# Kernel optimization log

Measured on AMD Instinct MI355X. Metric: run time of the kernel, lower is better.

Reference implementation:

```python
import jax, jax.numpy as jnp
import numpy as np

N_HEADS = 16
D_MODEL = 1024
TOTAL = 8192
N_SEQ = 8
SEQ_LEN = TOTAL // N_SEQ


def setup_inputs() -> dict:
    key = jax.random.key(0)
    ks = jax.random.split(key, 12)
    f = jnp.float32
    d = D_MODEL
    inp = {
        "query": jax.random.normal(ks[0], (TOTAL, d), f),
        "key": jax.random.normal(ks[1], (TOTAL, d), f),
        "value": jax.random.normal(ks[2], (TOTAL, d), f),
        "seq_lengths_q": jnp.full((N_SEQ,), SEQ_LEN, jnp.int64 if jax.config.jax_enable_x64 else jnp.int32),
        "seq_lengths_kv": jnp.full((N_SEQ,), SEQ_LEN, jnp.int64 if jax.config.jax_enable_x64 else jnp.int32),
        "Wq": jax.random.normal(ks[3], (d, d), f) * 0.02,
        "bq": jnp.zeros((d,), f),
        "Wk": jax.random.normal(ks[4], (d, d), f) * 0.02,
        "bk": jnp.zeros((d,), f),
        "Wv": jax.random.normal(ks[5], (d, d), f) * 0.02,
        "bv": jnp.zeros((d,), f),
        "Wo": jax.random.normal(ks[6], (d, d), f) * 0.02,
        "bo": jnpp if False else jnp.zeros((d,), f),
    }
    return inp


def reference(query, key, value, seq_lengths_q, seq_lengths_kv, Wq, bq, Wk, bk, Wv, bv, Wo, bo):
    Tq, d = query.shape
    Tkv = key.shape[0]
    H = N_HEADS
    Dh = d // H
    B = seq_lengths_q.shape[0]
    Lq = Tq // B  # equal-length packed sequences
    Lkv = Tkv // B
    scale = 1.0 / jnp.sqrt(jnp.asarray(Dh, query.dtype))

    # torch Linear: x @ W.T + b
    Q = (query @ Wq.T + bq).reshape(H, Tq, Dh)   # NOTE: raw view, no transpose
    K = (key @ Wk.T + bk).reshape(H, Tkv, Dh)    # (replicates original's view semantics)
    V = (value @ Wv.T + bv).reshape(H, Tkv, Dh)

    # Block-diagonal mask over equal-length sequences == per-block attention.
    Qb = Q.reshape(H, B, Lq, Dh)
    Kb = K.reshape(H, B, Lkv, Dh)
    Vb = V.reshape(H, B, Lkv, Dh)

    scores = jnp.einsum("hbqd,hbkd->hbqk", Qb, Kb) * scale  # [H,B,Lq,Lkv]
    probs = jax.nn.softmax(scores, axis=-1)
    attn = jnp.einsum("hbqk,hbkd->hbqd", probs, Vb)          # [H,B,Lq,Dh]

    attn = attn.reshape(H, Tq, Dh).reshape(Tq, d)  # matches .view(total_q, d_model)
    out = attn @ Wo.T + bo
    return out
```

## Files before the change

kernel.cpp:

```cpp
#include <hip/hip_runtime.h>
#include <hip/hip_bf16.h>

#define TOTAL   8192
#define DMODEL  1024
#define NHEADS  16
#define NSEQ    8
#define DH      64

typedef float  f32x4 __attribute__((ext_vector_type(4)));
typedef short  s16x8 __attribute__((ext_vector_type(8)));
typedef unsigned short u16;
typedef u16    u16x8 __attribute__((ext_vector_type(8)));

__device__ __forceinline__ u16 f2bf_rne(float x) {
  union { float f; unsigned u; } v; v.f = x;
  unsigned r = v.u + 0x7FFFu + ((v.u >> 16) & 1u);
  return (u16)(r >> 16);
}

__device__ __forceinline__ void async_cp16(const u16* g, u16* l) {
  __builtin_amdgcn_global_load_lds(
      (const __attribute__((address_space(1))) unsigned int*)g,
      (__attribute__((address_space(3))) unsigned int*)l, 16, 0, 0);
}

__device__ __forceinline__ void cvt8_one(const float* __restrict__ src,
                                         u16* __restrict__ dst, long i) {
  float4 a = *reinterpret_cast<const float4*>(src + i);
  float4 b = *reinterpret_cast<const float4*>(src + i + 4);
  u16x8 o;
  o[0] = f2bf_rne(a.x); o[1] = f2bf_rne(a.y); o[2] = f2bf_rne(a.z); o[3] = f2bf_rne(a.w);
  o[4] = f2bf_rne(b.x); o[5] = f2bf_rne(b.y); o[6] = f2bf_rne(b.z); o[7] = f2bf_rne(b.w);
  *reinterpret_cast<u16x8*>(dst + i) = o;
}

__global__ __launch_bounds__(256) void cvt8(const float* __restrict__ src,
                                            u16* __restrict__ dst) {
  cvt8_one(src, dst, ((long)blockIdx.x * 256 + threadIdx.x) * 8);
}

__global__ __launch_bounds__(256) void cvt8_w4(const float* __restrict__ w0,
                                               const float* __restrict__ w1,
                                               const float* __restrict__ w2,
                                               const float* __restrict__ w3,
                                               u16* __restrict__ dst) {
  const float* srcs[4] = {w0, w1, w2, w3};
  cvt8_one(srcs[blockIdx.y], dst + (long)blockIdx.y * (DMODEL * (long)DMODEL),
           ((long)blockIdx.x * 256 + threadIdx.x) * 8);
}

__global__ __launch_bounds__(256) void cvt8_x3(const float* __restrict__ x0,
                                               const float* __restrict__ x1,
                                               const float* __restrict__ x2,
                                               u16* __restrict__ dst) {
  const float* srcs[3] = {x0, x1, x2};
  cvt8_one(srcs[blockIdx.y], dst + (long)blockIdx.y * (TOTAL * (long)DMODEL),
           ((long)blockIdx.x * 256 + threadIdx.x) * 8);
}

template<bool OUT_BF16>
__device__ __forceinline__ void gemm_core(const u16* __restrict__ A,
                                          const u16* __restrict__ B,
                                          const float* __restrict__ bias,
                                          void* __restrict__ Cp,
                                          long bm0, long bn0,
                                          u16* As, u16* Bs) {
  const int tid  = threadIdx.x;
  const int lane = tid & 63;
  const int wv   = tid >> 6;
  const int quad = lane >> 4;
  const int m16  = lane & 15;
  const int wm   = (wv & 1) * 64;
  const int wn   = (wv >> 1) * 64;
  const int srow = lane >> 2;
  const int sk8  = (lane & 3) * 8;

  f32x4 acc[4][4] = {};
  const u16* Abase = A + bm0 * DMODEL;
  const u16* Bbase = B + bn0 * DMODEL;

  for (int k0 = 0; k0 < DMODEL; k0 += 32) {
    #pragma unroll
    for (int j = 0; j < 2; j++) {
      const int r   = j * 4 + wv;
      const int row = r * 16 + srow;
      async_cp16(Abase + (long)row * DMODEL + k0 + sk8, &As[r * 512]);
      async_cp16(Bbase + (long)row * DMODEL + k0 + sk8, &Bs[r * 512]);
    }
    __syncthreads();

    s16x8 af[4], bfr[4];
    #pragma unroll
    for (int i = 0; i < 4; i++)
      af[i] = *(const s16x8*)&As[(wm + i * 16 + m16) * 32 + quad * 8];
    #pragma unroll
    for (int j = 0; j < 4; j++)
      bfr[j] = *(const s16x8*)&Bs[(wn + j * 16 + m16) * 32 + quad * 8];
    #pragma unroll
    for (int i = 0; i < 4; i++)
      #pragma unroll
      for (int j = 0; j < 4; j++)
        acc[i][j] = __builtin_amdgcn_mfma_f32_16x16x32_bf16(af[i], bfr[j], acc[i][j], 0, 0, 0);
    __syncthreads();
  }

  #pragma unroll
  for (int j = 0; j < 4; j++) {
    const long col = bn0 + wn + j * 16 + m16;
    const float bj = bias[col];
    #pragma unroll
    for (int i = 0; i < 4; i++) {
      const long row0 = bm0 + wm + i * 16 + quad * 4;
      #pragma unroll
      for (int r = 0; r < 4; r++) {
        float v = acc[i][j][r] + bj;
        if constexpr (OUT_BF16)
          ((u16*)Cp)[(row0 + r) * DMODEL + col] = f2bf_rne(v);
        else
          ((float*)Cp)[(row0 + r) * DMODEL + col] = v;
      }
    }
  }
}

template<bool OUT_BF16>
__global__ __launch_bounds__(256) void gemm_nt_async(const u16* __restrict__ A,
                                                     const u16* __restrict__ B,
                                                     const float* __restrict__ bias,
                                                     void* __restrict__ Cp) {
  __shared__ u16 As[128 * 32];
  __shared__ u16 Bs[128 * 32];
  gemm_core<OUT_BF16>(A, B, bias, Cp,
                      (long)blockIdx.x * 128, (long)blockIdx.y * 128, As, Bs);
}

__global__ __launch_bounds__(256) void gemm_qkv(const u16* __restrict__ X3,
                                                const u16* __restrict__ W3,
                                                const float* __restrict__ bq,
                                                const float* __restrict__ bk,
                                                const float* __restrict__ bv,
                                                u16* __restrict__ QKV) {
  __shared__ u16 As[128 * 32];
  __shared__ u16 Bs[128 * 32];
  const int z = blockIdx.z;
  const float* bias = (z == 0) ? bq : (z == 1) ? bk : bv;
  gemm_core<true>(X3 + (long)z * (TOTAL * (long)DMODEL),
                  W3 + (long)z * (DMODEL * (long)DMODEL),
                  bias,
                  QKV + (long)z * (TOTAL * (long)DMODEL),
                  (long)blockIdx.x * 128, (long)blockIdx.y * 128, As, Bs);
}

__global__ __launch_bounds__(256) void transpose_v(const u16* __restrict__ Vbf,
                                                   u16* __restrict__ Vt) {
  constexpr int TP = 72;
  __shared__ u16 tile[64 * TP];
  const int tid = threadIdx.x;
  const long base = (long)blockIdx.y * 65536;
  const int kt = blockIdx.x;
  {
    int k = tid >> 2, dh0 = (tid & 3) * 16;
    const u16* g = Vbf + base + (long)(kt * 64 + k) * 64 + dh0;
    u16x8 a = ((const u16x8*)g)[0];
    u16x8 b = ((const u16x8*)g)[1];
    #pragma unroll
    for (int i = 0; i < 8; i++) tile[(dh0 + i) * TP + k] = a[i];
    #pragma unroll
    for (int i = 0; i < 8; i++) tile[(dh0 + 8 + i) * TP + k] = b[i];
  }
  __syncthreads();
  {
    int dh = tid >> 2, k0 = (tid & 3) * 16;
    u16x8 a = *(const u16x8*)&tile[dh * TP + k0];
    u16x8 b = *(const u16x8*)&tile[dh * TP + k0 + 8];
    u16* g = Vt + base + (long)dh * 1024 + kt * 64 + k0;
    ((u16x8*)g)[0] = a;
    ((u16x8*)g)[1] = b;
  }
}

__global__ __launch_bounds__(256) void attn_kernel(const u16* __restrict__ Qbf,
                                                   const u16* __restrict__ Kbf,
                                                   const u16* __restrict__ Vt,
                                                   u16* __restrict__ Obf) {
  constexpr int KP = 72;
  __shared__ u16 Ks[64 * KP];
  __shared__ u16 Vs[64 * KP];
  __shared__ u16 Es[4 * 32 * KP];
  const int tid  = threadIdx.x;
  const int lane = tid & 63;
  const int wv   = tid >> 6;
  const int quad = lane >> 4;
  const int m16  = lane & 15;
  const int qt   = blockIdx.y;
  const long base = (long)blockIdx.x * 65536;

  const int qrow0 = qt * 128 + wv * 32;
  s16x8 aq[2][2];
  #pragma unroll
  for (int g = 0; g < 2; g++)
    #pragma unroll
    for (int s = 0; s < 2; s++)
      aq[g][s] = *(const s16x8*)(Qbf + base + (long)(qrow0 + g * 16 + m16) * 64 + s * 32 + quad * 8);

  f32x4 acc_o[2][4] = {};
  f32x4 acc_d[2] = {};

  union { u16x8 u; s16x8 s; } onesu;
  u16 ov = (m16 == 0) ? (u16)0x3F80 : (u16)0;
  #pragma unroll
  for (int i = 0; i < 8; i++) onesu.u[i] = ov;
  const s16x8 bones = onesu.s;

  const float SC = 0.125f * 1.44269504088896340736f;
  const int sr = tid >> 2;
  const int sk = (tid & 3) * 16;

  for (int nt = 0; nt < 16; nt++) {
    {
      const u16* g = Kbf + base + nt * 4096 + (long)sr * 64 + sk;
      u16x8 a = ((const u16x8*)g)[0];
      u16x8 b = ((const u16x8*)g)[1];
      *(u16x8*)&Ks[sr * KP + sk]     = a;
      *(u16x8*)&Ks[sr * KP + sk + 8] = b;
    }
    {
      const u16* g = Vt + base + (long)sr * 1024 + nt * 64 + sk;
      u16x8 a = ((const u16x8*)g)[0];
      u16x8 b = ((const u16x8*)g)[1];
      *(u16x8*)&Vs[sr * KP + sk]     = a;
      *(u16x8*)&Vs[sr * KP + sk + 8] = b;
    }
    __syncthreads();

    #pragma unroll
    for (int n = 0; n < 4; n++) {
      s16x8 bk0 = *(const s16x8*)&Ks[(n * 16 + m16) * KP + quad * 8];
      s16x8 bk1 = *(const s16x8*)&Ks[(n * 16 + m16) * KP + 32 + quad * 8];
      #pragma unroll
      for (int g = 0; g < 2; g++) {
        f32x4 s = {0.f, 0.f, 0.f, 0.f};
        s = __builtin_amdgcn_mfma_f32_16x16x32_bf16(aq[g][0], bk0, s, 0, 0, 0);
        s = __builtin_amdgcn_mfma_f32_16x16x32_bf16(aq[g][1], bk1, s, 0, 0, 0);
        #pragma unroll
        for (int r = 0; r < 4; r++) {
          float e = __builtin_amdgcn_exp2f(s[r] * SC);
          Es[(wv * 32 + g * 16 + quad * 4 + r) * KP + n * 16 + m16] = f2bf_rne(e);
        }
      }
    }
    s16x8 ae[2][2];
    #pragma unroll
    for (int g = 0; g < 2; g++) {
      ae[g][0] = *(const s16x8*)&Es[(wv * 32 + g * 16 + m16) * KP + quad * 8];
      ae[g][1] = *(const s16x8*)&Es[(wv * 32 + g * 16 + m16) * KP + 32 + quad * 8];
    }
    #pragma unroll
    for (int n = 0; n < 4; n++) {
      s16x8 bv0 = *(const s16x8*)&Vs[(n * 16 + m16) * KP + quad * 8];
      s16x8 bv1 = *(const s16x8*)&Vs[(n * 16 + m16) * KP + 32 + quad * 8];
      #pragma unroll
      for (int g = 0; g < 2; g++) {
        acc_o[g][n] = __builtin_amdgcn_mfma_f32_16x16x32_bf16(ae[g][0], bv0, acc_o[g][n], 0, 0, 0);
        acc_o[g][n] = __builtin_amdgcn_mfma_f32_16x16x32_bf16(ae[g][1], bv1, acc_o[g][n], 0, 0, 0);
      }
    }
    #pragma unroll
    for (int g = 0; g < 2; g++) {
      acc_d[g] = __builtin_amdgcn_mfma_f32_16x16x32_bf16(ae[g][0], bones, acc_d[g], 0, 0, 0);
      acc_d[g] = __builtin_amdgcn_mfma_f32_16x16x32_bf16(ae[g][1], bones, acc_d[g], 0, 0, 0);
    }
    __syncthreads();
  }

  #pragma unroll
  for (int g = 0; g < 2; g++)
    #pragma unroll
    for (int r = 0; r < 4; r++) {
      float d = __shfl(acc_d[g][r], lane & 48);
      float rinv = 1.0f / d;
      const long orow = base + (long)(qrow0 + g * 16 + quad * 4 + r) * 64;
      #pragma unroll
      for (int n = 0; n < 4; n++)
        Obf[orow + n * 16 + m16] = f2bf_rne(acc_o[g][n][r] * rinv);
    }
}

extern "C" void kernel_launch(void* const* d_in, const int* in_sizes, int n_in,
                              void* d_out, int out_size, void* d_ws, size_t ws_size,
                              hipStream_t stream) {
  const float* query = (const float*)d_in[0];
  const float* key_  = (const float*)d_in[1];
  const float* value = (const float*)d_in[2];
  const float* Wq = (const float*)d_in[5];
  const float* bq = (const float*)d_in[6];
  const float* Wk = (const float*)d_in[7];
  const float* bk = (const float*)d_in[8];
  const float* Wv = (const float*)d_in[9];
  const float* bv = (const float*)d_in[10];
  const float* Wo = (const float*)d_in[11];
  const float* bo = (const float*)d_in[12];

  char* ws = (char*)d_ws;
  const size_t FUSED_NEED = 104ull << 20;

  if (ws_size >= FUSED_NEED) {
    u16* Wbf = (u16*)(ws);
    u16* QKV = (u16*)(ws + (8l << 20));
    u16* Qbf = QKV;
    u16* Kbf = QKV + 1 * (TOTAL * (long)DMODEL);
    u16* Vbf = QKV + 2 * (TOTAL * (long)DMODEL);
    u16* X3  = (u16*)(ws + (56l << 20));
    u16* Vt  = X3;
    u16* Obf = Vbf;

    cvt8_w4<<<dim3(512, 4), 256, 0, stream>>>(Wq, Wk, Wv, Wo, Wbf);
    cvt8_x3<<<dim3(4096, 3), 256, 0, stream>>>(query, key_, value, X3);
    gemm_qkv<<<dim3(64, 8, 3), 256, 0, stream>>>(X3, Wbf, bq, bk, bv, QKV);
    transpose_v<<<dim3(16, 128), 256, 0, stream>>>(Vbf, Vt);
    attn_kernel<<<dim3(128, 8), 256, 0, stream>>>(Qbf, Kbf, Vt, Obf);
    gemm_nt_async<false><<<dim3(64, 8), 256, 0, stream>>>(Obf, Wbf + 3 * 1048576, bo, (float*)d_out);
  } else {
    u16* Wbf = (u16*)(ws);
    u16* Xbf = (u16*)(ws + (8l << 20));
    u16* Qbf = (u16*)(ws + (24l << 20));
    u16* Kbf = (u16*)(ws + (40l << 20));
    u16* Vbf = (u16*)(ws + (56l << 20));
    u16* Vt  = Xbf;
    u16* Obf = Vbf;

    cvt8_w4<<<dim3(512, 4), 256, 0, stream>>>(Wq, Wk, Wv, Wo, Wbf);
    cvt8<<<4096, 256, 0, stream>>>(query, Xbf);
    gemm_nt_async<true><<<dim3(64, 8), 256, 0, stream>>>(Xbf, Wbf + 0 * 1048576, bq, Qbf);
    cvt8<<<4096, 256, 0, stream>>>(key_, Xbf);
    gemm_nt_async<true><<<dim3(64, 8), 256, 0, stream>>>(Xbf, Wbf + 1 * 1048576, bk, Kbf);
    cvt8<<<4096, 256, 0, stream>>>(value, Xbf);
    gemm_nt_async<true><<<dim3(64, 8), 256, 0, stream>>>(Xbf, Wbf + 2 * 1048576, bv, Vbf);
    transpose_v<<<dim3(16, 128), 256, 0, stream>>>(Vbf, Vt);
    attn_kernel<<<dim3(128, 8), 256, 0, stream>>>(Qbf, Kbf, Vt, Obf);
    gemm_nt_async<false><<<dim3(64, 8), 256, 0, stream>>>(Obf, Wbf + 3 * 1048576, bo, (float*)d_out);
  }
}
```

Before: 326.5 us.

## Fuse fp32-to-bf16 input conversion into QKV GEMM and deepen output GEMM K-tile

```diff
diff --git a/kernel.cpp b/kernel.cpp
--- a/kernel.cpp
+++ b/kernel.cpp
@@ -11,11 +11,18 @@
 typedef short  s16x8 __attribute__((ext_vector_type(8)));
 typedef unsigned short u16;
 typedef u16    u16x8 __attribute__((ext_vector_type(8)));
+typedef unsigned int u32;
+typedef u32    u32x4 __attribute__((ext_vector_type(4)));
 
 __device__ __forceinline__ u16 f2bf_rne(float x) {
   union { float f; unsigned u; } v; v.f = x;
   unsigned r = v.u + 0x7FFFu + ((v.u >> 16) & 1u);
   return (u16)(r >> 16);
+}
+
+__device__ __forceinline__ u32 pk_hu(float a, float b) {
+  union { float f; u32 u; } A, B; A.f = a; B.f = b;
+  return __builtin_amdgcn_perm(B.u + 0x8000u, A.u + 0x8000u, 0x07060302u);
 }
 
 __device__ __forceinline__ void async_cp16(const u16* g, u16* l) {
@@ -34,11 +41,6 @@
   *reinterpret_cast<u16x8*>(dst + i) = o;
 }
 
-__global__ __launch_bounds__(256) void cvt8(const float* __restrict__ src,
-                                            u16* __restrict__ dst) {
-  cvt8_one(src, dst, ((long)blockIdx.x * 256 + threadIdx.x) * 8);
-}
-
 __global__ __launch_bounds__(256) void cvt8_w4(const float* __restrict__ w0,
                                                const float* __restrict__ w1,
                                                const float* __restrict__ w2,
@@ -49,22 +51,22 @@
            ((long)blockIdx.x * 256 + threadIdx.x) * 8);
 }
 
-__global__ __launch_bounds__(256) void cvt8_x3(const float* __restrict__ x0,
-                                               const float* __restrict__ x1,
-                                               const float* __restrict__ x2,
-                                               u16* __restrict__ dst) {
-  const float* srcs[3] = {x0, x1, x2};
-  cvt8_one(srcs[blockIdx.y], dst + (long)blockIdx.y * (TOTAL * (long)DMODEL),
-           ((long)blockIdx.x * 256 + threadIdx.x) * 8);
-}
-
-template<bool OUT_BF16>
-__device__ __forceinline__ void gemm_core(const u16* __restrict__ A,
-                                          const u16* __restrict__ B,
-                                          const float* __restrict__ bias,
-                                          void* __restrict__ Cp,
-                                          long bm0, long bn0,
-                                          u16* As, u16* Bs) {
+__global__ __launch_bounds__(256) void gemm_qkv_f32a(const float* __restrict__ Xq,
+                                                     const float* __restrict__ Xk,
+                                                     const float* __restrict__ Xv,
+                                                     const u16*  __restrict__ W3,
+                                                     const float* __restrict__ bq,
+                                                     const float* __restrict__ bk,
+                                                     const float* __restrict__ bv,
+                                                     u16* __restrict__ QKV) {
+  __shared__ u16 As[128 * 32];
+  __shared__ u16 Bs[128 * 32];
+  const int z = blockIdx.z;
+  const float* X    = (z == 0) ? Xq : (z == 1) ? Xk : Xv;
+  const float* bias = (z == 0) ? bq : (z == 1) ? bk : bv;
+  const u16* B = W3 + (long)z * (DMODEL * (long)DMODEL);
+  u16* C = QKV + (long)z * (TOTAL * (long)DMODEL);
+
   const int tid  = threadIdx.x;
   const int lane = tid & 63;
   const int wv   = tid >> 6;
@@ -72,35 +74,114 @@
   const int m16  = lane & 15;
   const int wm   = (wv & 1) * 64;
   const int wn   = (wv >> 1) * 64;
+  const long bm0 = (long)blockIdx.x * 128;
+  const long bn0 = (long)blockIdx.y * 128;
+
+  const int arow = tid >> 1;
+  const int acol = (tid & 1) * 16;
   const int srow = lane >> 2;
   const int sk8  = (lane & 3) * 8;
+
+  f32x4 acc[4][4] = {};
+  const float* Abase = X + (bm0 + arow) * (long)DMODEL + acol;
+  const u16*   Bbase = B + bn0 * DMODEL;
+
+  for (int k0 = 0; k0 < DMODEL; k0 += 32) {
+    #pragma unroll
+    for (int j = 0; j < 2; j++) {
+      const int r = j * 4 + wv;
+      async_cp16(Bbase + (long)(r * 16 + srow) * DMODEL + k0 + sk8, &Bs[r * 512]);
+    }
+    {
+      const float4* ga = (const float4*)(Abase + k0);
+      float4 x0 = ga[0], x1 = ga[1], x2 = ga[2], x3 = ga[3];
+      u32x4 p0, p1;
+      p0[0] = pk_hu(x0.x, x0.y); p0[1] = pk_hu(x0.z, x0.w);
+      p0[2] = pk_hu(x1.x, x1.y); p0[3] = pk_hu(x1.z, x1.w);
+      p1[0] = pk_hu(x2.x, x2.y); p1[1] = pk_hu(x2.z, x2.w);
+      p1[2] = pk_hu(x3.x, x3.y); p1[3] = pk_hu(x3.z, x3.w);
+      *(u32x4*)&As[arow * 32 + acol]     = p0;
+      *(u32x4*)&As[arow * 32 + acol + 8] = p1;
+    }
+    __syncthreads();
+
+    s16x8 af[4], bfr[4];
+    #pragma unroll
+    for (int i = 0; i < 4; i++)
+      af[i] = *(const s16x8*)&As[(wm + i * 16 + m16) * 32 + quad * 8];
+    #pragma unroll
+    for (int j = 0; j < 4; j++)
+      bfr[j] = *(const s16x8*)&Bs[(wn + j * 16 + m16) * 32 + quad * 8];
+    #pragma unroll
+    for (int i = 0; i < 4; i++)
+      #pragma unroll
+      for (int j = 0; j < 4; j++)
+        acc[i][j] = __builtin_amdgcn_mfma_f32_16x16x32_bf16(af[i], bfr[j], acc[i][j], 0, 0, 0);
+    __syncthreads();
+  }
+
+  #pragma unroll
+  for (int j = 0; j < 4; j++) {
+    const long col = bn0 + wn + j * 16 + m16;
+    const float bj = bias[col];
+    #pragma unroll
+    for (int i = 0; i < 4; i++) {
+      const long row0 = bm0 + wm + i * 16 + quad * 4;
+      #pragma unroll
+      for (int r = 0; r < 4; r++)
+        C[(row0 + r) * DMODEL + col] = f2bf_rne(acc[i][j][r] + bj);
+    }
+  }
+}
+
+__global__ __launch_bounds__(256) void gemm_out64(const u16* __restrict__ A,
+                                                  const u16* __restrict__ B,
+                                                  const float* __restrict__ bias,
+                                                  float* __restrict__ C) {
+  __shared__ u16 As[128 * 64];
+  __shared__ u16 Bs[128 * 64];
+  const int tid  = threadIdx.x;
+  const int lane = tid & 63;
+  const int wv   = tid >> 6;
+  const int quad = lane >> 4;
+  const int m16  = lane & 15;
+  const int wm   = (wv & 1) * 64;
+  const int wn   = (wv >> 1) * 64;
+  const long bm0 = (long)blockIdx.x * 128;
+  const long bn0 = (long)blockIdx.y * 128;
+
+  const int r8 = lane >> 3;
+  const int c8 = (lane & 7) * 8;
 
   f32x4 acc[4][4] = {};
   const u16* Abase = A + bm0 * DMODEL;
   const u16* Bbase = B + bn0 * DMODEL;
 
-  for (int k0 = 0; k0 < DMODEL; k0 += 32) {
-    #pragma unroll
-    for (int j = 0; j < 2; j++) {
-      const int r   = j * 4 + wv;
-      const int row = r * 16 + srow;
-      async_cp16(Abase + (long)row * DMODEL + k0 + sk8, &As[r * 512]);
-      async_cp16(Bbase + (long)row * DMODEL + k0 + sk8, &Bs[r * 512]);
-    }
-    __syncthreads();
-
-    s16x8 af[4], bfr[4];
-    #pragma unroll
-    for (int i = 0; i < 4; i++)
-      af[i] = *(const s16x8*)&As[(wm + i * 16 + m16) * 32 + quad * 8];
-    #pragma unroll
-    for (int j = 0; j < 4; j++)
-      bfr[j] = *(const s16x8*)&Bs[(wn + j * 16 + m16) * 32 + quad * 8];
-    #pragma unroll
-    for (int i = 0; i < 4; i++)
+  for (int k0 = 0; k0 < DMODEL; k0 += 64) {
+    #pragma unroll
+    for (int j = 0; j < 4; j++) {
+      const int rr = j * 4 + wv;
+      const long row = rr * 8 + r8;
+      async_cp16(Abase + row * DMODEL + k0 + c8, &As[rr * 512]);
+      async_cp16(Bbase + row * DMODEL + k0 + c8, &Bs[rr * 512]);
+    }
+    __syncthreads();
+
+    #pragma unroll
+    for (int ks = 0; ks < 2; ks++) {
+      s16x8 af[4], bfr[4];
+      #pragma unroll
+      for (int i = 0; i < 4; i++)
+        af[i] = *(const s16x8*)&As[(wm + i * 16 + m16) * 64 + ks * 32 + quad * 8];
       #pragma unroll
       for (int j = 0; j < 4; j++)
-        acc[i][j] = __builtin_amdgcn_mfma_f32_16x16x32_bf16(af[i], bfr[j], acc[i][j], 0, 0, 0);
+        bfr[j] = *(const s16x8*)&Bs[(wn + j * 16 + m16) * 64 + ks * 32 + quad * 8];
+      #pragma unroll
+      for (int i = 0; i < 4; i++)
+        #pragma unroll
+        for (int j = 0; j < 4; j++)
+          acc[i][j] = __builtin_amdgcn_mfma_f32_16x16x32_bf16(af[i], bfr[j], acc[i][j], 0, 0, 0);
+    }
     __syncthreads();
   }
 
@@ -112,43 +193,10 @@
     for (int i = 0; i < 4; i++) {
       const long row0 = bm0 + wm + i * 16 + quad * 4;
       #pragma unroll
-      for (int r = 0; r < 4; r++) {
-        float v = acc[i][j][r] + bj;
-        if constexpr (OUT_BF16)
-          ((u16*)Cp)[(row0 + r) * DMODEL + col] = f2bf_rne(v);
-        else
-          ((float*)Cp)[(row0 + r) * DMODEL + col] = v;
-      }
-    }
-  }
-}
-
-template<bool OUT_BF16>
-__global__ __launch_bounds__(256) void gemm_nt_async(const u16* __restrict__ A,
-                                                     const u16* __restrict__ B,
-                                                     const float* __restrict__ bias,
-                                                     void* __restrict__ Cp) {
-  __shared__ u16 As[128 * 32];
-  __shared__ u16 Bs[128 * 32];
-  gemm_core<OUT_BF16>(A, B, bias, Cp,
-                      (long)blockIdx.x * 128, (long)blockIdx.y * 128, As, Bs);
-}
-
-__global__ __launch_bounds__(256) void gemm_qkv(const u16* __restrict__ X3,
-                                                const u16* __restrict__ W3,
-                                                const float* __restrict__ bq,
-                                                const float* __restrict__ bk,
-                                                const float* __restrict__ bv,
-                                                u16* __restrict__ QKV) {
-  __shared__ u16 As[128 * 32];
-  __shared__ u16 Bs[128 * 32];
-  const int z = blockIdx.z;
-  const float* bias = (z == 0) ? bq : (z == 1) ? bk : bv;
-  gemm_core<true>(X3 + (long)z * (TOTAL * (long)DMODEL),
-                  W3 + (long)z * (DMODEL * (long)DMODEL),
-                  bias,
-                  QKV + (long)z * (TOTAL * (long)DMODEL),
-                  (long)blockIdx.x * 128, (long)blockIdx.y * 128, As, Bs);
+      for (int r = 0; r < 4; r++)
+        C[(row0 + r) * DMODEL + col] = acc[i][j][r] + bj;
+    }
+  }
 }
 
 __global__ __launch_bounds__(256) void transpose_v(const u16* __restrict__ Vbf,
@@ -302,42 +350,18 @@
   const float* bo = (const float*)d_in[12];
 
   char* ws = (char*)d_ws;
-  const size_t FUSED_NEED = 104ull << 20;
-
-  if (ws_size >= FUSED_NEED) {
-    u16* Wbf = (u16*)(ws);
-    u16* QKV = (u16*)(ws + (8l << 20));
-    u16* Qbf = QKV;
-    u16* Kbf = QKV + 1 * (TOTAL * (long)DMODEL);
-    u16* Vbf = QKV + 2 * (TOTAL * (long)DMODEL);
-    u16* X3  = (u16*)(ws + (56l << 20));
-    u16* Vt  = X3;
-    u16* Obf = Vbf;
-
-    cvt8_w4<<<dim3(512, 4), 256, 0, stream>>>(Wq, Wk, Wv, Wo, Wbf);
-    cvt8_x3<<<dim3(4096, 3), 256, 0, stream>>>(query, key_, value, X3);
-    gemm_qkv<<<dim3(64, 8, 3), 256, 0, stream>>>(X3, Wbf, bq, bk, bv, QKV);
-    transpose_v<<<dim3(16, 128), 256, 0, stream>>>(Vbf, Vt);
-    attn_kernel<<<dim3(128, 8), 256, 0, stream>>>(Qbf, Kbf, Vt, Obf);
-    gemm_nt_async<false><<<dim3(64, 8), 256, 0, stream>>>(Obf, Wbf + 3 * 1048576, bo, (float*)d_out);
-  } else {
-    u16* Wbf = (u16*)(ws);
-    u16* Xbf = (u16*)(ws + (8l << 20));
-    u16* Qbf = (u16*)(ws + (24l << 20));
-    u16* Kbf = (u16*)(ws + (40l << 20));
-    u16* Vbf = (u16*)(ws + (56l << 20));
-    u16* Vt  = Xbf;
-    u16* Obf = Vbf;
-
-    cvt8_w4<<<dim3(512, 4), 256, 0, stream>>>(Wq, Wk, Wv, Wo, Wbf);
-    cvt8<<<4096, 256, 0, stream>>>(query, Xbf);
-    gemm_nt_async<true><<<dim3(64, 8), 256, 0, stream>>>(Xbf, Wbf + 0 * 1048576, bq, Qbf);
-    cvt8<<<4096, 256, 0, stream>>>(key_, Xbf);
-    gemm_nt_async<true><<<dim3(64, 8), 256, 0, stream>>>(Xbf, Wbf + 1 * 1048576, bk, Kbf);
-    cvt8<<<4096, 256, 0, stream>>>(value, Xbf);
-    gemm_nt_async<true><<<dim3(64, 8), 256, 0, stream>>>(Xbf, Wbf + 2 * 1048576, bv, Vbf);
-    transpose_v<<<dim3(16, 128), 256, 0, stream>>>(Vbf, Vt);
-    attn_kernel<<<dim3(128, 8), 256, 0, stream>>>(Qbf, Kbf, Vt, Obf);
-    gemm_nt_async<false><<<dim3(64, 8), 256, 0, stream>>>(Obf, Wbf + 3 * 1048576, bo, (float*)d_out);
-  }
-}
+  u16* Wbf = (u16*)(ws);
+  u16* QKV = (u16*)(ws + (8l << 20));
+  u16* Qbf = QKV;
+  u16* Kbf = QKV + 1 * (TOTAL * (long)DMODEL);
+  u16* Vbf = QKV + 2 * (TOTAL * (long)DMODEL);
+  u16* Vt  = (u16*)(ws + (56l << 20));
+  u16* Obf = Vbf;
+
+  cvt8_w4<<<dim3(512, 4), 256, 0, stream>>>(Wq, Wk, Wv, Wo, Wbf);
+  gemm_qkv_f32a<<<dim3(64, 8, 3), 256, 0, stream>>>(query, key_, value, Wbf,
+                                                    bq, bk, bv, QKV);
+  transpose_v<<<dim3(16, 128), 256, 0, stream>>>(Vbf, Vt);
+  attn_kernel<<<dim3(128, 8), 256, 0, stream>>>(Qbf, Kbf, Vt, Obf);
+  gemm_out64<<<dim3(64, 8), 256, 0, stream>>>(Obf, Wbf + 3 * 1048576, bo, (float*)d_out);
+}
```

New measurement: 349.8 us. +7.1%, slower.
